# Kernel optimization log

Measured on AMD Instinct MI355X. Metric: run time of the kernel, lower is better.

Reference implementation:

```python
import jax, jax.numpy as jnp
import numpy as np

B, C, H, W = 4, 3, 96, 96
HW = H * W
IGNORE = 0          # HD_IGNORE_CLASS_INDEX
BIG = 1e9           # stand-in for +inf in masked min


def setup_inputs() -> dict:
    key = jax.random.key(0)
    k1, k2 = jax.random.split(key)
    predictions = jax.random.normal(k1, (B, C, H, W), dtype=jnp.float32)
    labels_int = jax.random.randint(k2, (B, H, W), 0, C, dtype=jnp.int32)
    return {"predictions": predictions, "labels_int": labels_int}


def get_boundary(img):
    # img: [B, C, H, W] binary mask. Faithful to the numpy version (square images):
    # new = img + 4-neighbor sums (zero outside), boundary = img * (5 - new).
    pad = lambda x, spec: jnp.pad(x, ((0, 0), (0, 0)) + spec)
    new = (img
           + pad(img[:, :, 1:, :], ((0, 1), (0, 0)))
           + pad(img[:, :, :-1, :], ((1, 0), (0, 0)))
           + pad(img[:, :, :, 1:], ((0, 0), (0, 1)))
           + pad(img[:, :, :, :-1], ((0, 0), (1, 0))))
    return img * (5.0 - new)


def _pixel_dist_matrix():
    yy, xx = jnp.meshgrid(jnp.arange(H), jnp.arange(W), indexing="ij")
    coords = jnp.stack([yy.ravel(), xx.ravel()], axis=-1).astype(jnp.float32)  # [HW,2] (row,col) like argwhere
    sq = jnp.sum(coords * coords, axis=-1)
    D2 = sq[:, None] + sq[None, :] - 2.0 * (coords @ coords.T)
    return jnp.sqrt(jnp.maximum(D2, 0.0))  # [HW, HW]


def reference(predictions, labels_int):
    labels = jax.nn.one_hot(labels_int, C, axis=1, dtype=jnp.float32)        # [B,C,H,W]
    preds = jax.nn.one_hot(jnp.argmax(predictions, axis=1), C, axis=1,
                           dtype=jnp.float32)                                # [B,C,H,W]

    bd_a = (get_boundary(preds) > 0).astype(jnp.float32)
    bd_b = (get_boundary(labels) > 0).astype(jnp.float32)

    a = preds.reshape(B * C, HW)
    b = labels.reshape(B * C, HW)
    ba = bd_a.reshape(B * C, HW)
    bb = bd_b.reshape(B * C, HW)

    D = _pixel_dist_matrix()  # [HW, HW], shared across all (batch, class) pairs

    def pair(args):
        a_, b_, ba_, bb_ = args
        n_a = a_.sum()
        n_b = b_.sum()
        a_fwd = a_ * (1.0 - b_)   # pred-only pixels (false positive region)
        b_bwd = b_ * (1.0 - a_)   # label-only pixels
        # min distance from every pixel to boundary set, via masked min (no argwhere)
        mins_f = jnp.min(jnp.where(bb_[None, :] > 0, D, BIG), axis=1)  # to boundary(b)
        mins_b = jnp.min(jnp.where(ba_[None, :] > 0, D, BIG), axis=1)  # to boundary(a)
        # mean(min) * |A_fwd| / |a| == sum(min over A_fwd) / |a|
        hd_f = jnp.where((a_fwd.sum() > 0) & (bb_.sum() > 0),
                         jnp.sum(a_fwd * mins_f) / jnp.maximum(n_a, 1.0), 0.0)
        hd_b = jnp.where((b_bwd.sum() > 0) & (ba_.sum() > 0),
                         jnp.sum(b_bwd * mins_b) / jnp.maximum(n_b, 1.0), 0.0)
        hd = jnp.maximum(hd_f, hd_b)
        # empty prediction mask -> failure case (ignore_failed_hd = False => (h+w)/4)
        hd = jnp.where(n_a > 0, hd, (H + W) / 4.0)
        return hd, (n_a == 0).astype(jnp.float32)

    hd_pairs, failed_pairs = jax.lax.map(pair, (a, b, ba, bb))

    hd = hd_pairs.reshape(B, C).at[:, IGNORE].set(0.0)
    failed = failed_pairs.reshape(B, C).sum(axis=0).at[IGNORE].set(0.0)

    HD = jnp.zeros((B, C + 2), dtype=jnp.float32)
    HD = HD.at[:, :C].set(hd)
    HD = HD.at[:, C].set(jnp.mean(hd, axis=1))            # HD[:, -2] = mean over all C classes
    HD = HD.at[:, C + 1].set(jnp.mean(hd[:, :C - 1], axis=1))  # HD[:, -1] = mean over first C-1 (faithful to [:-3])

    Fc = jnp.zeros((C + 2,), dtype=jnp.float32)
    Fc = Fc.at[:C].set(failed)
    Fc = Fc.at[C].set(jnp.mean(failed))
    Fc = Fc.at[C + 1].set(jnp.mean(failed[1:C]))
    return HD, Fc
```

## Files before the change

### kernel.cpp

```cpp
#include <hip/hip_runtime.h>
#include <math.h>

namespace {
constexpr int Bn = 4, Cn = 3, Hn = 96, Wn = 96;
constexpr int HWn = Hn * Wn;
constexpr int NP  = Bn * Cn;
constexpr int STRIDE = 16;

constexpr int PC_OFF  = 0;
constexpr int CTR_OFF = Bn * HWn;
constexpr int CTR_WORDS = 4 * NP * STRIDE;
constexpr int BD_OFF  = CTR_OFF + CTR_WORDS;
constexpr int MK_OFF  = BD_OFF + NP * HWn;

constexpr int SENT = 62500;

__device__ __forceinline__ int CNT_NA_I(int pr) { return CTR_OFF + (0 * NP + pr) * STRIDE; }
__device__ __forceinline__ int CNT_NB_I(int pr) { return CTR_OFF + (1 * NP + pr) * STRIDE; }
__device__ __forceinline__ int SUM_F_I(int pr)  { return CTR_OFF + (2 * NP + pr) * STRIDE; }
__device__ __forceinline__ int SUM_B_I(int pr)  { return CTR_OFF + (3 * NP + pr) * STRIDE; }
}

__global__ void k_prep(const float* __restrict__ preds, int* __restrict__ wi) {
    int idx = blockIdx.x * blockDim.x + threadIdx.x;
    if (idx < CTR_WORDS) wi[CTR_OFF + idx] = 0;
    if (idx >= Bn * HWn) return;
    int b = idx / HWn, p = idx - b * HWn;
    const float* base = preds + (size_t)b * Cn * HWn + p;
    float best = base[0];
    int bi = 0;
#pragma unroll
    for (int c = 1; c < Cn; ++c) {
        float v = base[(size_t)c * HWn];
        if (v > best) { best = v; bi = c; }
    }
    wi[PC_OFF + idx] = bi;
}

__global__ void k_boundary(const int* __restrict__ labels, int* __restrict__ wi) {
    int idx = blockIdx.x * blockDim.x + threadIdx.x;
    int pr = idx / HWn, p = idx - pr * HWn;
    int b = pr / Cn, c = pr - b * Cn;
    int y = p / Wn, x = p - y * Wn;
    const int* pc = wi + PC_OFF + b * HWn;
    const int* lb = labels + b * HWn;
    int a  = (pc[p] == c);
    int bm = (lb[p] == c);

    int bda = 0, bdb = 0;
    if (a) {
        int cnt = 0;
        if (y > 0)      cnt += (pc[p - Wn] == c);
        if (y < Hn - 1) cnt += (pc[p + Wn] == c);
        if (x > 0)      cnt += (pc[p - 1] == c);
        if (x < Wn - 1) cnt += (pc[p + 1] == c);
        bda = (cnt < 4);
    }
    if (bm) {
        int cnt = 0;
        if (y > 0)      cnt += (lb[p - Wn] == c);
        if (y < Hn - 1) cnt += (lb[p + Wn] == c);
        if (x > 0)      cnt += (lb[p - 1] == c);
        if (x < Wn - 1) cnt += (lb[p + 1] == c);
        bdb = (cnt < 4);
    }
    wi[BD_OFF + pr * HWn + p] = bda | (bdb << 1);

    int lane = threadIdx.x & 63;
    unsigned long long ma = __ballot(a);
    unsigned long long mb = __ballot(bm);
    if (lane == 0) {
        if (ma) atomicAdd(&wi[CNT_NA_I(pr)], __popcll(ma));
        if (mb) atomicAdd(&wi[CNT_NB_I(pr)], __popcll(mb));
    }
}

__global__ void k_masks(int* __restrict__ wi) {
    int t = blockIdx.x * blockDim.x + threadIdx.x;
    if (t >= NP * 288) return;
    int pr = t / 288, rem = t - pr * 288;
    int w = rem / 96, x = rem - w * 96;
    const int* bd = wi + BD_OFF + pr * HWn;
    unsigned int am = 0, bm = 0;
#pragma unroll
    for (int k = 0; k < 32; ++k) {
        int f = bd[(w * 32 + k) * Wn + x];
        am |= (unsigned)(f & 1) << k;
        bm |= (unsigned)((f >> 1) & 1) << k;
    }
    wi[MK_OFF + pr * 576 + w * 96 + x]       = (int)am;
    wi[MK_OFF + pr * 576 + (w + 3) * 96 + x] = (int)bm;
}

__global__ void k_edt_sum(const int* __restrict__ labels,
                          const int* __restrict__ wi, float* __restrict__ wf) {
    int pr = blockIdx.y;
    int rb = blockIdx.x;
    int j  = threadIdx.x;
    int b = pr / Cn, c = pr - b * Cn;

    __shared__ unsigned int mlds[576];
    __shared__ unsigned int glds[384];

    for (int k = j; k < 576; k += 384)
        mlds[k] = (unsigned int)wi[MK_OFF + pr * 576 + k];
    __syncthreads();

    int r = j / 96, xp = j - r * 96;
    int y = rb * 4 + r;

    unsigned long long alo = (unsigned long long)mlds[xp]
                           | ((unsigned long long)mlds[96 + xp] << 32);
    unsigned long long ahi = mlds[192 + xp];
    unsigned long long blo = (unsigned long long)mlds[288 + xp]
                           | ((unsigned long long)mlds[384 + xp] << 32);
    unsigned long long bhi = mlds[480 + xp];

    __uint128_t Ma = ((__uint128_t)ahi << 64) | alo;
    __uint128_t Mb = ((__uint128_t)bhi << 64) | blo;

    auto dist1d = [&](__uint128_t M) -> int {
        int du = 200, dd = 200;
        __uint128_t s = M >> y;
        if (s) {
            unsigned long long l = (unsigned long long)s;
            du = l ? __builtin_ctzll(l) : 64 + __builtin_ctzll((unsigned long long)(s >> 64));
        }
        s = M << (127 - y);
        if (s) {
            unsigned long long h = (unsigned long long)(s >> 64);
            dd = h ? __builtin_clzll(h) : 64 + __builtin_clzll((unsigned long long)s);
        }
        int d = min(du, dd);
        return (d >= Hn) ? SENT : d * d;
    };
    glds[j] = (unsigned)dist1d(Mb) | ((unsigned)dist1d(Ma) << 16);
    __syncthreads();

    int x = xp, p = y * Wn + x;
    int a   = (wi[PC_OFF + b * HWn + p] == c);
    int bmf = (labels[b * HWn + p] == c);
    int na = wi[CNT_NA_I(pr)];
    int nb = wi[CNT_NB_I(pr)];
    bool af = a && !bmf && (nb > 0);
    bool bw = bmf && !a && (na > 0);

    float s = 0.0f;
    if (af || bw) {
        int sh = af ? 0 : 16;
        int md2 = 0x7fffffff;
        const unsigned int* grow = &glds[r * 96];
#pragma unroll 8
        for (int q = 0; q < Wn; ++q) {
            int gs = (grow[q] >> sh) & 0xffff;
            int dx = x - q;
            md2 = min(md2, gs + dx * dx);
        }
        s = sqrtf((float)md2);
    }
    float vF = af ? s : 0.0f;
    float vB = bw ? s : 0.0f;
#pragma unroll
    for (int off = 32; off >= 1; off >>= 1) {
        vF += __shfl_xor(vF, off, 64);
        vB += __shfl_xor(vB, off, 64);
    }
    if ((j & 63) == 0) {
        if (vF != 0.0f) atomicAdd(&wf[SUM_F_I(pr)], vF);
        if (vB != 0.0f) atomicAdd(&wf[SUM_B_I(pr)], vB);
    }
}

__global__ void k_final(const int* __restrict__ wi, const float* __restrict__ wf,
                        float* __restrict__ out) {
    if (blockIdx.x != 0 || threadIdx.x != 0) return;
    float hd[Bn][Cn];
    float failed[Cn] = {0.f, 0.f, 0.f};
    for (int pr = 0; pr < NP; ++pr) {
        int b = pr / Cn, c = pr - b * Cn;
        int na = wi[CNT_NA_I(pr)];
        int nb = wi[CNT_NB_I(pr)];
        float h;
        if (na == 0) {
            h = (Hn + Wn) / 4.0f;
            failed[c] += 1.0f;
        } else {
            float hf = wf[SUM_F_I(pr)] / fmaxf((float)na, 1.0f);
            float hb = wf[SUM_B_I(pr)] / fmaxf((float)nb, 1.0f);
            h = fmaxf(hf, hb);
        }
        if (c == 0) h = 0.0f;
        hd[b][c] = h;
    }
    failed[0] = 0.0f;
    for (int b = 0; b < Bn; ++b) {
        float* row = out + b * (Cn + 2);
        float s = 0.f;
        for (int c = 0; c < Cn; ++c) { row[c] = hd[b][c]; s += hd[b][c]; }
        row[Cn] = s / (float)Cn;
        row[Cn + 1] = (hd[b][0] + hd[b][1]) / (float)(Cn - 1);
    }
    float* Fc = out + Bn * (Cn + 2);
    float fs = 0.f;
    for (int c = 0; c < Cn; ++c) { Fc[c] = failed[c]; fs += failed[c]; }
    Fc[Cn] = fs / (float)Cn;
    Fc[Cn + 1] = (failed[1] + failed[2]) / (float)(Cn - 1);
}

extern "C" void kernel_launch(void* const* d_in, const int* in_sizes, int n_in,
                              void* d_out, int out_size, void* d_ws, size_t ws_size,
                              hipStream_t stream) {
    const float* preds  = (const float*)d_in[0];
    const int*   labels = (const int*)d_in[1];
    float* out = (float*)d_out;
    int*   wi = (int*)d_ws;
    float* wf = (float*)d_ws;

    k_prep<<<(Bn * HWn + 255) / 256, 256, 0, stream>>>(preds, wi);
    k_boundary<<<(NP * HWn) / 256, 256, 0, stream>>>(labels, wi);
    k_masks<<<(NP * 288 + 255) / 256, 256, 0, stream>>>(wi);
    dim3 g4(Hn / 4, NP);
    k_edt_sum<<<g4, 384, 0, stream>>>(labels, wi, wf);
    k_final<<<1, 64, 0, stream>>>(wi, wf, out);
}
```

Measured before the change: 77.65 us.

## Fuse argmax and boundary into one pass, fold final reduction into EDT kernel

Merges the argmax and boundary kernels into a single front kernel. It recomputes neighbour argmaxes and packs the pred class, label class and both boundary bits into one byte per pixel for every class at once. Per-block class counts replace global atomics and are reduced in the mask kernel. A last-block ticket at the end of the EDT kernel does the final output math, cutting two launches. The cost is redundant argmax reads and a threadfence/atomic ticket.

```diff
diff --git a/kernel.cpp b/kernel.cpp
--- a/kernel.cpp
+++ b/kernel.cpp
@@ -5,95 +5,97 @@
 constexpr int Bn = 4, Cn = 3, Hn = 96, Wn = 96;
 constexpr int HWn = Hn * Wn;
 constexpr int NP  = Bn * Cn;
-constexpr int STRIDE = 16;
-
-constexpr int PC_OFF  = 0;
-constexpr int CTR_OFF = Bn * HWn;
-constexpr int CTR_WORDS = 4 * NP * STRIDE;
-constexpr int BD_OFF  = CTR_OFF + CTR_WORDS;
-constexpr int MK_OFF  = BD_OFF + NP * HWn;
-
+constexpr int NBLK1 = (Bn * HWn) / 256;
 constexpr int SENT = 62500;
 
-__device__ __forceinline__ int CNT_NA_I(int pr) { return CTR_OFF + (0 * NP + pr) * STRIDE; }
-__device__ __forceinline__ int CNT_NB_I(int pr) { return CTR_OFF + (1 * NP + pr) * STRIDE; }
-__device__ __forceinline__ int SUM_F_I(int pr)  { return CTR_OFF + (2 * NP + pr) * STRIDE; }
-__device__ __forceinline__ int SUM_B_I(int pr)  { return CTR_OFF + (3 * NP + pr) * STRIDE; }
-}
-
-__global__ void k_prep(const float* __restrict__ preds, int* __restrict__ wi) {
-    int idx = blockIdx.x * blockDim.x + threadIdx.x;
-    if (idx < CTR_WORDS) wi[CTR_OFF + idx] = 0;
-    if (idx >= Bn * HWn) return;
-    int b = idx / HWn, p = idx - b * HWn;
-    const float* base = preds + (size_t)b * Cn * HWn + p;
-    float best = base[0];
-    int bi = 0;
+constexpr int FLAG_WORDS = Bn * HWn / 4;
+constexpr int CNT_OFF  = FLAG_WORDS;
+constexpr int NA_OFF   = CNT_OFF + NBLK1 * 8;
+constexpr int NB_OFF   = NA_OFF + NP;
+constexpr int SUMF_OFF = NB_OFF + NP;
+constexpr int SUMB_OFF = SUMF_OFF + NP;
+constexpr int TICK_OFF = SUMB_OFF + NP + 4;
+constexpr int MK_OFF   = TICK_OFF + 12;
+}
+
+__global__ __launch_bounds__(256) void k_front(const float* __restrict__ preds,
+                                               const int* __restrict__ labels,
+                                               int* __restrict__ wi) {
+    int blk = blockIdx.x, tid = threadIdx.x;
+    int b = blk / 36;
+    int p = (blk - b * 36) * 256 + tid;
+    int y = p / Wn, x = p - y * Wn;
+    const float* pb = preds + (size_t)b * Cn * HWn;
+    const int*   lb = labels + b * HWn;
+
+    auto amax = [&](int q) -> int {
+        float v0 = pb[q], v1 = pb[HWn + q], v2 = pb[2 * HWn + q];
+        int bi = 0; float bv = v0;
+        if (v1 > bv) { bv = v1; bi = 1; }
+        if (v2 > bv) { bv = v2; bi = 2; }
+        return bi;
+    };
+    int pc = amax(p);
+    int l  = lb[p];
+    int ca = 0, cb = 0;
+    if (y > 0)      { ca += (amax(p - Wn) == pc); cb += (lb[p - Wn] == l); }
+    if (y < Hn - 1) { ca += (amax(p + Wn) == pc); cb += (lb[p + Wn] == l); }
+    if (x > 0)      { ca += (amax(p - 1)  == pc); cb += (lb[p - 1]  == l); }
+    if (x < Wn - 1) { ca += (amax(p + 1)  == pc); cb += (lb[p + 1]  == l); }
+    ((unsigned char*)wi)[b * HWn + p] =
+        (unsigned char)(pc | (l << 2) | ((ca < 4) << 4) | ((cb < 4) << 5));
+
+    __shared__ int wcnt[4][6];
+    int wv = tid >> 6, ln = tid & 63;
+    int cnts[6];
 #pragma unroll
-    for (int c = 1; c < Cn; ++c) {
-        float v = base[(size_t)c * HWn];
-        if (v > best) { best = v; bi = c; }
-    }
-    wi[PC_OFF + idx] = bi;
-}
-
-__global__ void k_boundary(const int* __restrict__ labels, int* __restrict__ wi) {
-    int idx = blockIdx.x * blockDim.x + threadIdx.x;
-    int pr = idx / HWn, p = idx - pr * HWn;
-    int b = pr / Cn, c = pr - b * Cn;
-    int y = p / Wn, x = p - y * Wn;
-    const int* pc = wi + PC_OFF + b * HWn;
-    const int* lb = labels + b * HWn;
-    int a  = (pc[p] == c);
-    int bm = (lb[p] == c);
-
-    int bda = 0, bdb = 0;
-    if (a) {
-        int cnt = 0;
-        if (y > 0)      cnt += (pc[p - Wn] == c);
-        if (y < Hn - 1) cnt += (pc[p + Wn] == c);
-        if (x > 0)      cnt += (pc[p - 1] == c);
-        if (x < Wn - 1) cnt += (pc[p + 1] == c);
-        bda = (cnt < 4);
-    }
-    if (bm) {
-        int cnt = 0;
-        if (y > 0)      cnt += (lb[p - Wn] == c);
-        if (y < Hn - 1) cnt += (lb[p + Wn] == c);
-        if (x > 0)      cnt += (lb[p - 1] == c);
-        if (x < Wn - 1) cnt += (lb[p + 1] == c);
-        bdb = (cnt < 4);
-    }
-    wi[BD_OFF + pr * HWn + p] = bda | (bdb << 1);
-
-    int lane = threadIdx.x & 63;
-    unsigned long long ma = __ballot(a);
-    unsigned long long mb = __ballot(bm);
-    if (lane == 0) {
-        if (ma) atomicAdd(&wi[CNT_NA_I(pr)], __popcll(ma));
-        if (mb) atomicAdd(&wi[CNT_NB_I(pr)], __popcll(mb));
+    for (int c = 0; c < 3; ++c) {
+        cnts[c]     = __popcll(__ballot(pc == c));
+        cnts[3 + c] = __popcll(__ballot(l == c));
+    }
+    if (ln == 0) {
+        for (int k = 0; k < 6; ++k) wcnt[wv][k] = cnts[k];
+    }
+    __syncthreads();
+    if (tid < 6)
+        wi[CNT_OFF + blk * 8 + tid] = wcnt[0][tid] + wcnt[1][tid] + wcnt[2][tid] + wcnt[3][tid];
+    if (blk == 0) {
+        if (tid < 24) wi[SUMF_OFF + tid] = 0;
+        if (tid == 24) wi[TICK_OFF] = 0;
     }
 }
 
 __global__ void k_masks(int* __restrict__ wi) {
     int t = blockIdx.x * blockDim.x + threadIdx.x;
-    if (t >= NP * 288) return;
-    int pr = t / 288, rem = t - pr * 288;
-    int w = rem / 96, x = rem - w * 96;
-    const int* bd = wi + BD_OFF + pr * HWn;
-    unsigned int am = 0, bm = 0;
+    const unsigned char* flags = (const unsigned char*)wi;
+    if (t < NP * 288) {
+        int b = t / 864, rem = t - b * 864;
+        int c = rem / 288, rem2 = rem - c * 288;
+        int w = rem2 / 96, x = rem2 - w * 96;
+        const unsigned char* fb = flags + b * HWn + x;
+        unsigned am = 0, bm = 0;
 #pragma unroll
-    for (int k = 0; k < 32; ++k) {
-        int f = bd[(w * 32 + k) * Wn + x];
-        am |= (unsigned)(f & 1) << k;
-        bm |= (unsigned)((f >> 1) & 1) << k;
-    }
-    wi[MK_OFF + pr * 576 + w * 96 + x]       = (int)am;
-    wi[MK_OFF + pr * 576 + (w + 3) * 96 + x] = (int)bm;
-}
-
-__global__ void k_edt_sum(const int* __restrict__ labels,
-                          const int* __restrict__ wi, float* __restrict__ wf) {
+        for (int k = 0; k < 32; ++k) {
+            unsigned f = fb[(w * 32 + k) * Wn];
+            am |= (unsigned)(((f >> 4) & 1) & (unsigned)((f & 3) == (unsigned)c)) << k;
+            bm |= (unsigned)(((f >> 5) & 1) & (unsigned)(((f >> 2) & 3) == (unsigned)c)) << k;
+        }
+        int pr = b * Cn + c;
+        wi[MK_OFF + pr * 576 + w * 96 + x]       = (int)am;
+        wi[MK_OFF + pr * 576 + (w + 3) * 96 + x] = (int)bm;
+    } else if (t < NP * 288 + 24) {
+        int idx = t - NP * 288;
+        int pr = idx % 12, which = idx / 12;
+        int b = pr / Cn, c = pr - b * Cn;
+        int s = 0;
+        for (int k = 0; k < 36; ++k) s += wi[CNT_OFF + (b * 36 + k) * 8 + which * 3 + c];
+        wi[(which ? NB_OFF : NA_OFF) + pr] = s;
+    }
+}
+
+__global__ __launch_bounds__(384) void k_edt_sum(int* __restrict__ wi,
+                                                 float* __restrict__ wf,
+                                                 float* __restrict__ out) {
     int pr = blockIdx.y;
     int rb = blockIdx.x;
     int j  = threadIdx.x;
@@ -101,6 +103,7 @@
 
     __shared__ unsigned int mlds[576];
     __shared__ unsigned int glds[384];
+    __shared__ int lastflag;
 
     for (int k = j; k < 576; k += 384)
         mlds[k] = (unsigned int)wi[MK_OFF + pr * 576 + k];
@@ -123,8 +126,8 @@
         int du = 200, dd = 200;
         __uint128_t s = M >> y;
         if (s) {
-            unsigned long long l = (unsigned long long)s;
-            du = l ? __builtin_ctzll(l) : 64 + __builtin_ctzll((unsigned long long)(s >> 64));
+            unsigned long long lo = (unsigned long long)s;
+            du = lo ? __builtin_ctzll(lo) : 64 + __builtin_ctzll((unsigned long long)(s >> 64));
         }
         s = M << (127 - y);
         if (s) {
@@ -137,13 +140,14 @@
     glds[j] = (unsigned)dist1d(Mb) | ((unsigned)dist1d(Ma) << 16);
     __syncthreads();
 
-    int x = xp, p = y * Wn + x;
-    int a   = (wi[PC_OFF + b * HWn + p] == c);
-    int bmf = (labels[b * HWn + p] == c);
-    int na = wi[CNT_NA_I(pr)];
-    int nb = wi[CNT_NB_I(pr)];
-    bool af = a && !bmf && (nb > 0);
-    bool bw = bmf && !a && (na > 0);
+    int p = y * Wn + xp;
+    unsigned f = ((const unsigned char*)wi)[b * HWn + p];
+    int a  = ((f & 3) == (unsigned)c);
+    int bm = (((f >> 2) & 3) == (unsigned)c);
+    int na = wi[NA_OFF + pr];
+    int nb = wi[NB_OFF + pr];
+    bool af = a && !bm && (nb > 0);
+    bool bw = bm && !a && (na > 0);
 
     float s = 0.0f;
     if (af || bw) {
@@ -153,7 +157,7 @@
 #pragma unroll 8
         for (int q = 0; q < Wn; ++q) {
             int gs = (grow[q] >> sh) & 0xffff;
-            int dx = x - q;
+            int dx = xp - q;
             md2 = min(md2, gs + dx * dx);
         }
         s = sqrtf((float)md2);
@@ -166,45 +170,52 @@
         vB += __shfl_xor(vB, off, 64);
     }
     if ((j & 63) == 0) {
-        if (vF != 0.0f) atomicAdd(&wf[SUM_F_I(pr)], vF);
-        if (vB != 0.0f) atomicAdd(&wf[SUM_B_I(pr)], vB);
-    }
-}
-
-__global__ void k_final(const int* __restrict__ wi, const float* __restrict__ wf,
-                        float* __restrict__ out) {
-    if (blockIdx.x != 0 || threadIdx.x != 0) return;
-    float hd[Bn][Cn];
-    float failed[Cn] = {0.f, 0.f, 0.f};
-    for (int pr = 0; pr < NP; ++pr) {
-        int b = pr / Cn, c = pr - b * Cn;
-        int na = wi[CNT_NA_I(pr)];
-        int nb = wi[CNT_NB_I(pr)];
-        float h;
-        if (na == 0) {
-            h = (Hn + Wn) / 4.0f;
-            failed[c] += 1.0f;
-        } else {
-            float hf = wf[SUM_F_I(pr)] / fmaxf((float)na, 1.0f);
-            float hb = wf[SUM_B_I(pr)] / fmaxf((float)nb, 1.0f);
-            h = fmaxf(hf, hb);
-        }
-        if (c == 0) h = 0.0f;
-        hd[b][c] = h;
-    }
-    failed[0] = 0.0f;
-    for (int b = 0; b < Bn; ++b) {
-        float* row = out + b * (Cn + 2);
-        float s = 0.f;
-        for (int c = 0; c < Cn; ++c) { row[c] = hd[b][c]; s += hd[b][c]; }
-        row[Cn] = s / (float)Cn;
-        row[Cn + 1] = (hd[b][0] + hd[b][1]) / (float)(Cn - 1);
-    }
-    float* Fc = out + Bn * (Cn + 2);
-    float fs = 0.f;
-    for (int c = 0; c < Cn; ++c) { Fc[c] = failed[c]; fs += failed[c]; }
-    Fc[Cn] = fs / (float)Cn;
-    Fc[Cn + 1] = (failed[1] + failed[2]) / (float)(Cn - 1);
+        if (vF != 0.0f) atomicAdd(&wf[SUMF_OFF + pr], vF);
+        if (vB != 0.0f) atomicAdd(&wf[SUMB_OFF + pr], vB);
+    }
+
+    __syncthreads();
+    if (j == 0) {
+        __threadfence();
+        int old = atomicAdd(&wi[TICK_OFF], 1);
+        lastflag = (old == NP * 24 - 1);
+    }
+    __syncthreads();
+    if (!lastflag) return;
+    __threadfence();
+
+    __shared__ float hds[12];
+    __shared__ float fld[12];
+    if (j < 12) {
+        int nA = wi[NA_OFF + j];
+        int nB = wi[NB_OFF + j];
+        float sF = atomicAdd(&wf[SUMF_OFF + j], 0.0f);
+        float sB = atomicAdd(&wf[SUMB_OFF + j], 0.0f);
+        float h, fl = 0.0f;
+        if (nA == 0) { h = (Hn + Wn) / 4.0f; fl = 1.0f; }
+        else {
+            h = fmaxf(sF / fmaxf((float)nA, 1.0f), sB / fmaxf((float)nB, 1.0f));
+        }
+        if (j % Cn == 0) { h = 0.0f; fl = 0.0f; }
+        hds[j] = h; fld[j] = fl;
+    }
+    __syncthreads();
+    if (j == 0) {
+        float failed[3] = {0.f, 0.f, 0.f};
+        for (int q = 0; q < 12; ++q) failed[q % 3] += fld[q];
+        for (int bb = 0; bb < Bn; ++bb) {
+            float* row = out + bb * (Cn + 2);
+            float ssum = 0.f;
+            for (int cc = 0; cc < Cn; ++cc) { row[cc] = hds[bb * 3 + cc]; ssum += row[cc]; }
+            row[Cn]     = ssum / (float)Cn;
+            row[Cn + 1] = (hds[bb * 3] + hds[bb * 3 + 1]) / (float)(Cn - 1);
+        }
+        float* Fc = out + Bn * (Cn + 2);
+        float fs = 0.f;
+        for (int cc = 0; cc < Cn; ++cc) { Fc[cc] = failed[cc]; fs += failed[cc]; }
+        Fc[Cn]     = fs / (float)Cn;
+        Fc[Cn + 1] = (failed[1] + failed[2]) / (float)(Cn - 1);
+    }
 }
 
 extern "C" void kernel_launch(void* const* d_in, const int* in_sizes, int n_in,
@@ -216,10 +227,8 @@
     int*   wi = (int*)d_ws;
     float* wf = (float*)d_ws;
 
-    k_prep<<<(Bn * HWn + 255) / 256, 256, 0, stream>>>(preds, wi);
-    k_boundary<<<(NP * HWn) / 256, 256, 0, stream>>>(labels, wi);
-    k_masks<<<(NP * 288 + 255) / 256, 256, 0, stream>>>(wi);
-    dim3 g4(Hn / 4, NP);
-    k_edt_sum<<<g4, 384, 0, stream>>>(labels, wi, wf);
-    k_final<<<1, 64, 0, stream>>>(wi, wf, out);
-}
+    k_front<<<NBLK1, 256, 0, stream>>>(preds, labels, wi);
+    k_masks<<<(NP * 288 + 24 + 255) / 256, 256, 0, stream>>>(wi);
+    dim3 g3(Hn / 4, NP);
+    k_edt_sum<<<g3, 384, 0, stream>>>(wi, wf, out);
+}
```

Result: slower. 98.60 us (+27.0%).
